# Performance work log

Hardware: AMD Instinct MI355X
Metric: run time of the kernel (lower is better)

## Reference

```python
import jax, jax.numpy as jnp
import numpy as np

DECAY = 0.1  # P['decay']


def setup_inputs() -> dict:
    key = jax.random.key(0)
    k0, k1, k2, k3, k4 = jax.random.split(key, 5)
    N, B, T = 512, 64, 1024
    hidden_0 = jax.random.normal(k0, (N,), dtype=jnp.float32)
    Batch_Input = jax.random.normal(k1, (B, T, N), dtype=jnp.float32)
    # scale recurrent weight ~1/sqrt(N) so the leaky-tanh dynamics stay bounded
    W = jax.random.normal(k2, (N, N), dtype=jnp.float32) / np.sqrt(N).astype(np.float32)
    Gw = jax.random.normal(k3, (2, N), dtype=jnp.float32)
    Gb = jax.random.normal(k4, (2,), dtype=jnp.float32)
    return {"hidden_0": hidden_0, "Batch_Input": Batch_Input, "W": W, "Gw": Gw, "Gb": Gb}


def reference(hidden_0, Batch_Input, W, Gw, Gb):
    B, T, N = Batch_Input.shape
    h0 = jnp.broadcast_to(hidden_0[None, :], (B, N))  # repeat over batch
    xs = jnp.swapaxes(Batch_Input, 0, 1)  # [T, B, N] for scan over time

    def step(h, x):
        # h_new = (1-d)*h + d*(tanh(h) @ W^T + x)   (einsum 'ab,cb->ca')
        h_new = (1.0 - DECAY) * h + DECAY * (jnp.tanh(h) @ W.T + x)
        return h_new, jnp.tanh(h_new)

    _, hidden_t = jax.lax.scan(step, h0, xs)  # hidden_t: [T, B, N]
    geometry = hidden_t @ Gw.T + Gb  # [T, B, 2]
    return jnp.swapaxes(hidden_t, 0, 1), jnp.swapaxes(geometry, 0, 1)
```

## Files before the change

### kernel.cpp

```cpp
#include <hip/hip_runtime.h>
#include <hip/hip_fp16.h>
#include <cmath>

#define RN 512
#define RT 1024
#define RB 64
#define SMEM_BYTES (131072 + 320)

typedef _Float16 half2v __attribute__((ext_vector_type(2)));

__device__ __forceinline__ float fast_tanh(float x) {
    float e = __expf(2.0f * x);
    return 1.0f - 2.0f / (e + 1.0f);
}
__device__ __forceinline__ unsigned pack2(float a, float b) {
    return (unsigned)__half_as_ushort(__float2half(a)) |
           ((unsigned)__half_as_ushort(__float2half(b)) << 16);
}
__device__ __forceinline__ unsigned pkrtz(float a, float b) {
    auto h = __builtin_amdgcn_cvt_pkrtz(a, b);
    return __builtin_bit_cast(unsigned, h);
}
__device__ __forceinline__ float dot2(unsigned wa, unsigned tb, float acc) {
    half2v a = __builtin_bit_cast(half2v, wa);
    half2v b = __builtin_bit_cast(half2v, tb);
    return __builtin_amdgcn_fdot2(a, b, acc, false);
}
template <int CTRL>
__device__ __forceinline__ float dpp_add(float x) {
    int p = __builtin_amdgcn_update_dpp(0, __float_as_int(x), CTRL, 0xf, 0xf, true);
    return x + __int_as_float(p);
}
__device__ __forceinline__ float red16(float x) {
    x = dpp_add<0xB1>(x);
    x = dpp_add<0x4E>(x);
    x = dpp_add<0x141>(x);
    x = dpp_add<0x140>(x);
    return x;
}
#define D2Q(acc, wq, tq) \
    acc = dot2((wq).x, (tq).x, acc); acc = dot2((wq).y, (tq).y, acc); \
    acc = dot2((wq).z, (tq).z, acc); acc = dot2((wq).w, (tq).w, acc);

__global__ void __launch_bounds__(512, 1) rnn_step_kernel(
    const float* __restrict__ h0,
    const float* __restrict__ X,
    const uint4* __restrict__ Wpk,
    const float* __restrict__ tanh0,
    float* __restrict__ outH,
    unsigned* __restrict__ ctr,
    unsigned* __restrict__ xcdctr)
{
    extern __shared__ unsigned char smem[];
    uint4*    Wl    = (uint4*)smem;
    unsigned* ownpk = (unsigned*)(smem + 131072);
    int*      bc    = (int*)(smem + 131072 + 256);
    unsigned* lctr  = (unsigned*)(smem + 131072 + 264);

    const int tid = threadIdx.x;
    if (tid == 0) {
        unsigned xcd;
        asm volatile("s_getreg_b32 %0, hwreg(HW_REG_XCC_ID)" : "=s"(xcd));
        xcd &= 7u;
        unsigned rank = __hip_atomic_fetch_add(&xcdctr[xcd], 1u,
                            __ATOMIC_RELAXED, __HIP_MEMORY_SCOPE_AGENT) & 31u;
        int slot = (int)(xcd * 32u + rank);
        bc[0] = slot >> 2;
        bc[1] = slot & 3;
        *lctr = 0u;
    }
    __syncthreads();
    const int batch = bc[0], part = bc[1];

    {
        const uint4* src = Wpk + part * 8192;
        #pragma unroll
        for (int i = 0; i < 16; ++i)
            Wl[i * 512 + tid] = src[i * 512 + tid];
    }

    const int rg = tid >> 4;
    const int kc = tid & 15;
    const int row0 = part * 128 + rg * 4;

    float4 h = {0, 0, 0, 0};
    float4 xv = {0, 0, 0, 0};
    if (kc == 0) {
        h = *reinterpret_cast<const float4*>(h0 + row0);
        float t0 = tanhf(h.x), t1 = tanhf(h.y), t2 = tanhf(h.z), t3 = tanhf(h.w);
        ownpk[2 * rg]     = pack2(t0, t1);
        ownpk[2 * rg + 1] = pack2(t2, t3);
        xv = *reinterpret_cast<const float4*>(&X[(size_t)batch * RT * RN + row0]);
    }

    unsigned* gctr = ctr + batch * 32;
    __syncthreads();

    #pragma unroll 1
    for (int t = 0; t < RT; ++t) {
        float4 xn = {0, 0, 0, 0};
        if (kc == 0) {
            const int tn = (t + 1 < RT) ? t + 1 : t;
            xn = *reinterpret_cast<const float4*>(&X[((size_t)batch * RT + tn) * RN + row0]);
        }

        float acc0 = 0.f, acc1 = 0.f, acc2 = 0.f, acc3 = 0.f;
        {
            uint4 th = *reinterpret_cast<const uint4*>(&ownpk[4 * kc]);
            uint4 wq0 = Wl[(part * 4 + 0) * 512 + tid];
            uint4 wq1 = Wl[(part * 4 + 1) * 512 + tid];
            uint4 wq2 = Wl[(part * 4 + 2) * 512 + tid];
            uint4 wq3 = Wl[(part * 4 + 3) * 512 + tid];
            D2Q(acc0, wq0, th) D2Q(acc1, wq1, th)
            D2Q(acc2, wq2, th) D2Q(acc3, wq3, th)
        }

        if (tid == 0 && t > 0) {
            const unsigned tgt = 4u * (unsigned)t;
            while (__hip_atomic_load(gctr, __ATOMIC_RELAXED,
                                     __HIP_MEMORY_SCOPE_AGENT) < tgt)
                __builtin_amdgcn_s_sleep(1);
        }
        __syncthreads();

        const float* srcR = (t == 0) ? tanh0
            : &outH[((size_t)batch * RT + (t - 1)) * RN];
        #pragma unroll
        for (int bb = 0; bb < 3; ++bb) {
            const int b = bb + (bb >= part);
            const int ko = b * 128 + kc * 8;
            float4 f0 = *reinterpret_cast<const float4*>(srcR + ko);
            float4 f1 = *reinterpret_cast<const float4*>(srcR + ko + 4);
            uint4 tv = make_uint4(pkrtz(f0.x, f0.y), pkrtz(f0.z, f0.w),
                                  pkrtz(f1.x, f1.y), pkrtz(f1.z, f1.w));
            uint4 wq0 = Wl[(b * 4 + 0) * 512 + tid];
            uint4 wq1 = Wl[(b * 4 + 1) * 512 + tid];
            uint4 wq2 = Wl[(b * 4 + 2) * 512 + tid];
            uint4 wq3 = Wl[(b * 4 + 3) * 512 + tid];
            D2Q(acc0, wq0, tv) D2Q(acc1, wq1, tv)
            D2Q(acc2, wq2, tv) D2Q(acc3, wq3, tv)
        }

        acc0 = red16(acc0); acc1 = red16(acc1);
        acc2 = red16(acc2); acc3 = red16(acc3);

        if (kc == 0) {
            h.x = 0.9f * h.x + 0.1f * (acc0 + xv.x);
            h.y = 0.9f * h.y + 0.1f * (acc1 + xv.y);
            h.z = 0.9f * h.z + 0.1f * (acc2 + xv.z);
            h.w = 0.9f * h.w + 0.1f * (acc3 + xv.w);
            float t0 = fast_tanh(h.x), t1 = fast_tanh(h.y);
            float t2 = fast_tanh(h.z), t3 = fast_tanh(h.w);
            *reinterpret_cast<float4*>(&outH[((size_t)batch * RT + t) * RN + row0]) =
                make_float4(t0, t1, t2, t3);
            ownpk[2 * rg]     = pack2(t0, t1);
            ownpk[2 * rg + 1] = pack2(t2, t3);
        }

        asm volatile("s_waitcnt vmcnt(0)" ::: "memory");
        if ((tid & 63) == 0) {
            unsigned a = __hip_atomic_fetch_add(lctr, 1u, __ATOMIC_RELAXED,
                                                __HIP_MEMORY_SCOPE_WORKGROUP);
            if ((a & 7u) == 7u)
                __hip_atomic_fetch_add(gctr, 1u, __ATOMIC_RELAXED,
                                       __HIP_MEMORY_SCOPE_AGENT);
        }
        __syncthreads();
        xv = xn;
    }
}

__global__ void pack_w(const float* __restrict__ W, uint4* __restrict__ Wpk)
{
    int o = blockIdx.x * blockDim.x + threadIdx.x;
    if (o >= 32768) return;
    int part = o >> 13;
    int b    = (o >> 11) & 3;
    int i    = (o >> 9) & 3;
    int tid  = o & 511;
    int row  = part * 128 + (tid >> 4) * 4 + i;
    int k0   = b * 128 + (tid & 15) * 8;
    const float* s = W + (size_t)row * RN + k0;
    uint4 v;
    v.x = pack2(s[0], s[1]); v.y = pack2(s[2], s[3]);
    v.z = pack2(s[4], s[5]); v.w = pack2(s[6], s[7]);
    Wpk[o] = v;
}

__global__ void geom_kernel(const float* __restrict__ hid,
                            const float* __restrict__ Gw,
                            const float* __restrict__ Gb,
                            float* __restrict__ geo)
{
    const int wid  = (blockIdx.x * blockDim.x + threadIdx.x) >> 6;
    const int lane = threadIdx.x & 63;
    if (wid >= RB * RT) return;
    const float* rowp = hid + (size_t)wid * RN;
    float g0 = 0.f, g1 = 0.f;
    #pragma unroll
    for (int j = 0; j < 8; ++j) {
        float v = rowp[lane + 64 * j];
        g0 = fmaf(v, Gw[lane + 64 * j], g0);
        g1 = fmaf(v, Gw[RN + lane + 64 * j], g1);
    }
    #pragma unroll
    for (int m = 32; m >= 1; m >>= 1) {
        g0 += __shfl_xor(g0, m);
        g1 += __shfl_xor(g1, m);
    }
    if (lane == 0) {
        geo[(size_t)wid * 2]     = g0 + Gb[0];
        geo[(size_t)wid * 2 + 1] = g1 + Gb[1];
    }
}

__global__ void init_misc(const float* __restrict__ h0,
                          float* __restrict__ tanh0,
                          unsigned* __restrict__ ctr,
                          unsigned* __restrict__ xcdctr)
{
    int i = blockIdx.x * blockDim.x + threadIdx.x;
    if (i < RN) tanh0[i] = tanhf(h0[i]);
    if (i < RB * 32) ctr[i] = 0u;
    if (i < 8) xcdctr[i] = 0u;
}

extern "C" void kernel_launch(void* const* d_in, const int* in_sizes, int n_in,
                              void* d_out, int out_size, void* d_ws, size_t ws_size,
                              hipStream_t stream)
{
    const float* h0 = (const float*)d_in[0];
    const float* X  = (const float*)d_in[1];
    const float* W  = (const float*)d_in[2];
    const float* Gw = (const float*)d_in[3];
    const float* Gb = (const float*)d_in[4];

    float* outH = (float*)d_out;
    float* geo  = outH + (size_t)RB * RT * RN;

    float*    tanh0  = (float*)d_ws;
    unsigned* ctr    = (unsigned*)d_ws + RN;
    unsigned* xcdctr = ctr + RB * 32;
    uint4*    Wpk    = (uint4*)(((uintptr_t)(xcdctr + 8) + 15) & ~(uintptr_t)15);

    (void)hipFuncSetAttribute((const void*)rnn_step_kernel,
                              hipFuncAttributeMaxDynamicSharedMemorySize, SMEM_BYTES);

    pack_w<<<64, 512, 0, stream>>>(W, Wpk);
    init_misc<<<8, 512, 0, stream>>>(h0, tanh0, ctr, xcdctr);

    void* kargs[] = { (void*)&h0, (void*)&X, (void*)&Wpk, (void*)&tanh0,
                      (void*)&outH, (void*)&ctr, (void*)&xcdctr };
    (void)hipLaunchCooperativeKernel(rnn_step_kernel, dim3(256), dim3(512),
                                     kargs, SMEM_BYTES, stream);

    geom_kernel<<<(RB * RT * 64 + 255) / 256, 256, 0, stream>>>(outH, Gw, Gb, geo);
}
```

Measured before the change: 2.034 ms.

## Process two batch rows per workgroup to reuse LDS weights and halve active blocks

Each workgroup now advances two batch sequences (b and b+32) at once, reusing each loaded weight fragment from LDS for two dot products. Only 16 of 32 launched blocks per XCD do work and the rest exit early, so 128 workgroups cover the 64 batches. This is meant to amortise LDS weight reads and the per-step barrier and spin-wait over twice the work. The cost is more compute, global loads and register pressure per step on each workgroup, plus reliance on the per-XCD rank assignment producing a valid mapping.

New measurement: 3.084 ms. +51.6%, slower.

```diff
diff --git a/kernel.cpp b/kernel.cpp
--- a/kernel.cpp
+++ b/kernel.cpp
@@ -5,7 +5,7 @@
 #define RN 512
 #define RT 1024
 #define RB 64
-#define SMEM_BYTES (131072 + 320)
+#define SMEM_BYTES (131072 + 1024)
 
 typedef _Float16 half2v __attribute__((ext_vector_type(2)));
 
@@ -54,8 +54,8 @@
     extern __shared__ unsigned char smem[];
     uint4*    Wl    = (uint4*)smem;
     unsigned* ownpk = (unsigned*)(smem + 131072);
-    int*      bc    = (int*)(smem + 131072 + 256);
-    unsigned* lctr  = (unsigned*)(smem + 131072 + 264);
+    int*      bc    = (int*)(smem + 131072 + 512);
+    unsigned* lctr  = (unsigned*)(smem + 131072 + 528);
 
     const int tid = threadIdx.x;
     if (tid == 0) {
@@ -64,13 +64,20 @@
         xcd &= 7u;
         unsigned rank = __hip_atomic_fetch_add(&xcdctr[xcd], 1u,
                             __ATOMIC_RELAXED, __HIP_MEMORY_SCOPE_AGENT) & 31u;
-        int slot = (int)(xcd * 32u + rank);
-        bc[0] = slot >> 2;
-        bc[1] = slot & 3;
+        if (rank < 16u) {
+            int slot = (int)(xcd * 16u + rank);
+            bc[0] = slot >> 2;
+            bc[1] = slot & 3;
+            bc[2] = 1;
+        } else {
+            bc[2] = 0;
+        }
         *lctr = 0u;
     }
     __syncthreads();
-    const int batch = bc[0], part = bc[1];
+    if (bc[2] == 0) return;
+    const int pair = bc[0], part = bc[1];
+    const int bA = pair, bB = pair + 32;
 
     {
         const uint4* src = Wpk + part * 8192;
@@ -83,36 +90,43 @@
     const int kc = tid & 15;
     const int row0 = part * 128 + rg * 4;
 
-    float4 h = {0, 0, 0, 0};
-    float4 xv = {0, 0, 0, 0};
+    float4 hA = {0,0,0,0}, hB = {0,0,0,0};
+    float4 xvA = {0,0,0,0}, xvB = {0,0,0,0};
     if (kc == 0) {
-        h = *reinterpret_cast<const float4*>(h0 + row0);
-        float t0 = tanhf(h.x), t1 = tanhf(h.y), t2 = tanhf(h.z), t3 = tanhf(h.w);
-        ownpk[2 * rg]     = pack2(t0, t1);
-        ownpk[2 * rg + 1] = pack2(t2, t3);
-        xv = *reinterpret_cast<const float4*>(&X[(size_t)batch * RT * RN + row0]);
-    }
-
-    unsigned* gctr = ctr + batch * 32;
+        hA = *reinterpret_cast<const float4*>(h0 + row0);
+        hB = hA;
+        float t0 = tanhf(hA.x), t1 = tanhf(hA.y), t2 = tanhf(hA.z), t3 = tanhf(hA.w);
+        ownpk[2 * rg]          = pack2(t0, t1);
+        ownpk[2 * rg + 1]      = pack2(t2, t3);
+        ownpk[64 + 2 * rg]     = pack2(t0, t1);
+        ownpk[64 + 2 * rg + 1] = pack2(t2, t3);
+        xvA = *reinterpret_cast<const float4*>(&X[(size_t)bA * RT * RN + row0]);
+        xvB = *reinterpret_cast<const float4*>(&X[(size_t)bB * RT * RN + row0]);
+    }
+
+    unsigned* gctr = ctr + pair * 32;
     __syncthreads();
 
     #pragma unroll 1
     for (int t = 0; t < RT; ++t) {
-        float4 xn = {0, 0, 0, 0};
+        float4 xnA = {0,0,0,0}, xnB = {0,0,0,0};
         if (kc == 0) {
             const int tn = (t + 1 < RT) ? t + 1 : t;
-            xn = *reinterpret_cast<const float4*>(&X[((size_t)batch * RT + tn) * RN + row0]);
-        }
-
-        float acc0 = 0.f, acc1 = 0.f, acc2 = 0.f, acc3 = 0.f;
+            xnA = *reinterpret_cast<const float4*>(&X[((size_t)bA * RT + tn) * RN + row0]);
+            xnB = *reinterpret_cast<const float4*>(&X[((size_t)bB * RT + tn) * RN + row0]);
+        }
+
+        float aA0 = 0.f, aA1 = 0.f, aA2 = 0.f, aA3 = 0.f;
+        float aB0 = 0.f, aB1 = 0.f, aB2 = 0.f, aB3 = 0.f;
         {
-            uint4 th = *reinterpret_cast<const uint4*>(&ownpk[4 * kc]);
+            uint4 thA = *reinterpret_cast<const uint4*>(&ownpk[4 * kc]);
+            uint4 thB = *reinterpret_cast<const uint4*>(&ownpk[64 + 4 * kc]);
             uint4 wq0 = Wl[(part * 4 + 0) * 512 + tid];
             uint4 wq1 = Wl[(part * 4 + 1) * 512 + tid];
             uint4 wq2 = Wl[(part * 4 + 2) * 512 + tid];
             uint4 wq3 = Wl[(part * 4 + 3) * 512 + tid];
-            D2Q(acc0, wq0, th) D2Q(acc1, wq1, th)
-            D2Q(acc2, wq2, th) D2Q(acc3, wq3, th)
+            D2Q(aA0, wq0, thA) D2Q(aA1, wq1, thA) D2Q(aA2, wq2, thA) D2Q(aA3, wq3, thA)
+            D2Q(aB0, wq0, thB) D2Q(aB1, wq1, thB) D2Q(aB2, wq2, thB) D2Q(aB3, wq3, thB)
         }
 
         if (tid == 0 && t > 0) {
@@ -123,38 +137,52 @@
         }
         __syncthreads();
 
-        const float* srcR = (t == 0) ? tanh0
-            : &outH[((size_t)batch * RT + (t - 1)) * RN];
+        const float* srcA = (t == 0) ? tanh0 : &outH[((size_t)bA * RT + (t - 1)) * RN];
+        const float* srcB = (t == 0) ? tanh0 : &outH[((size_t)bB * RT + (t - 1)) * RN];
         #pragma unroll
         for (int bb = 0; bb < 3; ++bb) {
             const int b = bb + (bb >= part);
             const int ko = b * 128 + kc * 8;
-            float4 f0 = *reinterpret_cast<const float4*>(srcR + ko);
-            float4 f1 = *reinterpret_cast<const float4*>(srcR + ko + 4);
-            uint4 tv = make_uint4(pkrtz(f0.x, f0.y), pkrtz(f0.z, f0.w),
-                                  pkrtz(f1.x, f1.y), pkrtz(f1.z, f1.w));
+            float4 fA0 = *reinterpret_cast<const float4*>(srcA + ko);
+            float4 fA1 = *reinterpret_cast<const float4*>(srcA + ko + 4);
+            float4 fB0 = *reinterpret_cast<const float4*>(srcB + ko);
+            float4 fB1 = *reinterpret_cast<const float4*>(srcB + ko + 4);
+            uint4 tvA = make_uint4(pkrtz(fA0.x, fA0.y), pkrtz(fA0.z, fA0.w),
+                                   pkrtz(fA1.x, fA1.y), pkrtz(fA1.z, fA1.w));
+            uint4 tvB = make_uint4(pkrtz(fB0.x, fB0.y), pkrtz(fB0.z, fB0.w),
+                                   pkrtz(fB1.x, fB1.y), pkrtz(fB1.z, fB1.w));
             uint4 wq0 = Wl[(b * 4 + 0) * 512 + tid];
             uint4 wq1 = Wl[(b * 4 + 1) * 512 + tid];
             uint4 wq2 = Wl[(b * 4 + 2) * 512 + tid];
             uint4 wq3 = Wl[(b * 4 + 3) * 512 + tid];
-            D2Q(acc0, wq0, tv) D2Q(acc1, wq1, tv)
-            D2Q(acc2, wq2, tv) D2Q(acc3, wq3, tv)
-        }
-
-        acc0 = red16(acc0); acc1 = red16(acc1);
-        acc2 = red16(acc2); acc3 = red16(acc3);
+            D2Q(aA0, wq0, tvA) D2Q(aA1, wq1, tvA) D2Q(aA2, wq2, tvA) D2Q(aA3, wq3, tvA)
+            D2Q(aB0, wq0, tvB) D2Q(aB1, wq1, tvB) D2Q(aB2, wq2, tvB) D2Q(aB3, wq3, tvB)
+        }
+
+        aA0 = red16(aA0); aA1 = red16(aA1); aA2 = red16(aA2); aA3 = red16(aA3);
+        aB0 = red16(aB0); aB1 = red16(aB1); aB2 = red16(aB2); aB3 = red16(aB3);
 
         if (kc == 0) {
-            h.x = 0.9f * h.x + 0.1f * (acc0 + xv.x);
-            h.y = 0.9f * h.y + 0.1f * (acc1 + xv.y);
-            h.z = 0.9f * h.z + 0.1f * (acc2 + xv.z);
-            h.w = 0.9f * h.w + 0.1f * (acc3 + xv.w);
-            float t0 = fast_tanh(h.x), t1 = fast_tanh(h.y);
-            float t2 = fast_tanh(h.z), t3 = fast_tanh(h.w);
-            *reinterpret_cast<float4*>(&outH[((size_t)batch * RT + t) * RN + row0]) =
-                make_float4(t0, t1, t2, t3);
-            ownpk[2 * rg]     = pack2(t0, t1);
-            ownpk[2 * rg + 1] = pack2(t2, t3);
+            hA.x = 0.9f * hA.x + 0.1f * (aA0 + xvA.x);
+            hA.y = 0.9f * hA.y + 0.1f * (aA1 + xvA.y);
+            hA.z = 0.9f * hA.z + 0.1f * (aA2 + xvA.z);
+            hA.w = 0.9f * hA.w + 0.1f * (aA3 + xvA.w);
+            hB.x = 0.9f * hB.x + 0.1f * (aB0 + xvB.x);
+            hB.y = 0.9f * hB.y + 0.1f * (aB1 + xvB.y);
+            hB.z = 0.9f * hB.z + 0.1f * (aB2 + xvB.z);
+            hB.w = 0.9f * hB.w + 0.1f * (aB3 + xvB.w);
+            float a0 = fast_tanh(hA.x), a1 = fast_tanh(hA.y);
+            float a2 = fast_tanh(hA.z), a3 = fast_tanh(hA.w);
+            float b0 = fast_tanh(hB.x), b1 = fast_tanh(hB.y);
+            float b2 = fast_tanh(hB.z), b3 = fast_tanh(hB.w);
+            *reinterpret_cast<float4*>(&outH[((size_t)bA * RT + t) * RN + row0]) =
+                make_float4(a0, a1, a2, a3);
+            *reinterpret_cast<float4*>(&outH[((size_t)bB * RT + t) * RN + row0]) =
+                make_float4(b0, b1, b2, b3);
+            ownpk[2 * rg]          = pack2(a0, a1);
+            ownpk[2 * rg + 1]      = pack2(a2, a3);
+            ownpk[64 + 2 * rg]     = pack2(b0, b1);
+            ownpk[64 + 2 * rg + 1] = pack2(b2, b3);
         }
 
         asm volatile("s_waitcnt vmcnt(0)" ::: "memory");
@@ -166,7 +194,7 @@
                                        __HIP_MEMORY_SCOPE_AGENT);
         }
         __syncthreads();
-        xv = xn;
+        xvA = xnA; xvB = xnB;
     }
 }
 
@@ -221,7 +249,7 @@
 {
     int i = blockIdx.x * blockDim.x + threadIdx.x;
     if (i < RN) tanh0[i] = tanhf(h0[i]);
-    if (i < RB * 32) ctr[i] = 0u;
+    if (i < 32 * 32) ctr[i] = 0u;
     if (i < 8) xcdctr[i] = 0u;
 }
 
@@ -240,7 +268,7 @@
 
     float*    tanh0  = (float*)d_ws;
     unsigned* ctr    = (unsigned*)d_ws + RN;
-    unsigned* xcdctr = ctr + RB * 32;
+    unsigned* xcdctr = ctr + 32 * 32;
     uint4*    Wpk    = (uint4*)(((uintptr_t)(xcdctr + 8) + 15) & ~(uintptr_t)15);
 
     (void)hipFuncSetAttribute((const void*)rnn_step_kernel,
```

## Switch recurrent matvec to column split with partial-sum exchange across blocks

Applied to the files above, without the earlier changes.

The recurrent matvec now gives each block a 128-column slice of W for all 512 output rows, using the block's own tanh values. Before, each block owned 128 rows and had to read the other blocks' tanh outputs after a barrier. Each block sends partial sums for the other blocks' rows through a double-buffered global exchange buffer, then reduces its own rows after the per-batch barrier. This removes the cross-lane DPP reduction and the dependent global reads of the other quarters' state before the matvec. It adds a global write and read of partial sums on every step and leaves only 64 threads to do the final update.

Result: slower. 2.540 ms (+24.9%).

```diff
diff --git a/kernel.cpp b/kernel.cpp
--- a/kernel.cpp
+++ b/kernel.cpp
@@ -5,7 +5,7 @@
 #define RN 512
 #define RT 1024
 #define RB 64
-#define SMEM_BYTES (131072 + 320)
+#define SMEM_BYTES 131872
 
 typedef _Float16 half2v __attribute__((ext_vector_type(2)));
 
@@ -16,28 +16,12 @@
 __device__ __forceinline__ unsigned pack2(float a, float b) {
     return (unsigned)__half_as_ushort(__float2half(a)) |
            ((unsigned)__half_as_ushort(__float2half(b)) << 16);
-}
-__device__ __forceinline__ unsigned pkrtz(float a, float b) {
-    auto h = __builtin_amdgcn_cvt_pkrtz(a, b);
-    return __builtin_bit_cast(unsigned, h);
 }
 __device__ __forceinline__ float dot2(unsigned wa, unsigned tb, float acc) {
     half2v a = __builtin_bit_cast(half2v, wa);
     half2v b = __builtin_bit_cast(half2v, tb);
     return __builtin_amdgcn_fdot2(a, b, acc, false);
 }
-template <int CTRL>
-__device__ __forceinline__ float dpp_add(float x) {
-    int p = __builtin_amdgcn_update_dpp(0, __float_as_int(x), CTRL, 0xf, 0xf, true);
-    return x + __int_as_float(p);
-}
-__device__ __forceinline__ float red16(float x) {
-    x = dpp_add<0xB1>(x);
-    x = dpp_add<0x4E>(x);
-    x = dpp_add<0x141>(x);
-    x = dpp_add<0x140>(x);
-    return x;
-}
 #define D2Q(acc, wq, tq) \
     acc = dot2((wq).x, (tq).x, acc); acc = dot2((wq).y, (tq).y, acc); \
     acc = dot2((wq).z, (tq).z, acc); acc = dot2((wq).w, (tq).w, acc);
@@ -46,16 +30,17 @@
     const float* __restrict__ h0,
     const float* __restrict__ X,
     const uint4* __restrict__ Wpk,
-    const float* __restrict__ tanh0,
     float* __restrict__ outH,
+    unsigned long long* __restrict__ exch,
     unsigned* __restrict__ ctr,
     unsigned* __restrict__ xcdctr)
 {
     extern __shared__ unsigned char smem[];
-    uint4*    Wl    = (uint4*)smem;
-    unsigned* ownpk = (unsigned*)(smem + 131072);
-    int*      bc    = (int*)(smem + 131072 + 256);
-    unsigned* lctr  = (unsigned*)(smem + 131072 + 264);
+    uint4*    Wl      = (uint4*)smem;
+    unsigned* ownpk   = (unsigned*)(smem + 131072);
+    float*    ownpart = (float*)(smem + 131072 + 256);
+    int*      bc      = (int*)(smem + 131072 + 768);
+    unsigned* lctr    = (unsigned*)(smem + 131072 + 776);
 
     const int tid = threadIdx.x;
     if (tid == 0) {
@@ -79,18 +64,12 @@
             Wl[i * 512 + tid] = src[i * 512 + tid];
     }
 
-    const int rg = tid >> 4;
-    const int kc = tid & 15;
-    const int row0 = part * 128 + rg * 4;
-
-    float4 h = {0, 0, 0, 0};
-    float4 xv = {0, 0, 0, 0};
-    if (kc == 0) {
-        h = *reinterpret_cast<const float4*>(h0 + row0);
-        float t0 = tanhf(h.x), t1 = tanhf(h.y), t2 = tanhf(h.z), t3 = tanhf(h.w);
-        ownpk[2 * rg]     = pack2(t0, t1);
-        ownpk[2 * rg + 1] = pack2(t2, t3);
-        xv = *reinterpret_cast<const float4*>(&X[(size_t)batch * RT * RN + row0]);
+    float2 hreg = {0.f, 0.f}, xv = {0.f, 0.f};
+    if (tid < 64) {
+        hreg = *reinterpret_cast<const float2*>(h0 + part * 128 + 2 * tid);
+        ownpk[tid] = pack2(tanhf(hreg.x), tanhf(hreg.y));
+        xv = *reinterpret_cast<const float2*>(
+            X + (size_t)batch * RT * RN + part * 128 + 2 * tid);
     }
 
     unsigned* gctr = ctr + batch * 32;
@@ -98,63 +77,38 @@
 
     #pragma unroll 1
     for (int t = 0; t < RT; ++t) {
-        float4 xn = {0, 0, 0, 0};
-        if (kc == 0) {
+        float2 xn = {0.f, 0.f};
+        if (tid < 64) {
             const int tn = (t + 1 < RT) ? t + 1 : t;
-            xn = *reinterpret_cast<const float4*>(&X[((size_t)batch * RT + tn) * RN + row0]);
-        }
-
-        float acc0 = 0.f, acc1 = 0.f, acc2 = 0.f, acc3 = 0.f;
+            xn = *reinterpret_cast<const float2*>(
+                X + ((size_t)batch * RT + tn) * RN + part * 128 + 2 * tid);
+        }
+
+        float acc = 0.f;
         {
-            uint4 th = *reinterpret_cast<const uint4*>(&ownpk[4 * kc]);
-            uint4 wq0 = Wl[(part * 4 + 0) * 512 + tid];
-            uint4 wq1 = Wl[(part * 4 + 1) * 512 + tid];
-            uint4 wq2 = Wl[(part * 4 + 2) * 512 + tid];
-            uint4 wq3 = Wl[(part * 4 + 3) * 512 + tid];
-            D2Q(acc0, wq0, th) D2Q(acc1, wq1, th)
-            D2Q(acc2, wq2, th) D2Q(acc3, wq3, th)
-        }
-
-        if (tid == 0 && t > 0) {
-            const unsigned tgt = 4u * (unsigned)t;
-            while (__hip_atomic_load(gctr, __ATOMIC_RELAXED,
-                                     __HIP_MEMORY_SCOPE_AGENT) < tgt)
-                __builtin_amdgcn_s_sleep(1);
-        }
-        __syncthreads();
-
-        const float* srcR = (t == 0) ? tanh0
-            : &outH[((size_t)batch * RT + (t - 1)) * RN];
-        #pragma unroll
-        for (int bb = 0; bb < 3; ++bb) {
-            const int b = bb + (bb >= part);
-            const int ko = b * 128 + kc * 8;
-            float4 f0 = *reinterpret_cast<const float4*>(srcR + ko);
-            float4 f1 = *reinterpret_cast<const float4*>(srcR + ko + 4);
-            uint4 tv = make_uint4(pkrtz(f0.x, f0.y), pkrtz(f0.z, f0.w),
-                                  pkrtz(f1.x, f1.y), pkrtz(f1.z, f1.w));
-            uint4 wq0 = Wl[(b * 4 + 0) * 512 + tid];
-            uint4 wq1 = Wl[(b * 4 + 1) * 512 + tid];
-            uint4 wq2 = Wl[(b * 4 + 2) * 512 + tid];
-            uint4 wq3 = Wl[(b * 4 + 3) * 512 + tid];
-            D2Q(acc0, wq0, tv) D2Q(acc1, wq1, tv)
-            D2Q(acc2, wq2, tv) D2Q(acc3, wq3, tv)
-        }
-
-        acc0 = red16(acc0); acc1 = red16(acc1);
-        acc2 = red16(acc2); acc3 = red16(acc3);
-
-        if (kc == 0) {
-            h.x = 0.9f * h.x + 0.1f * (acc0 + xv.x);
-            h.y = 0.9f * h.y + 0.1f * (acc1 + xv.y);
-            h.z = 0.9f * h.z + 0.1f * (acc2 + xv.z);
-            h.w = 0.9f * h.w + 0.1f * (acc3 + xv.w);
-            float t0 = fast_tanh(h.x), t1 = fast_tanh(h.y);
-            float t2 = fast_tanh(h.z), t3 = fast_tanh(h.w);
-            *reinterpret_cast<float4*>(&outH[((size_t)batch * RT + t) * RN + row0]) =
-                make_float4(t0, t1, t2, t3);
-            ownpk[2 * rg]     = pack2(t0, t1);
-            ownpk[2 * rg + 1] = pack2(t2, t3);
+            const uint4* wb = Wl + tid;
+            const uint4* tb = (const uint4*)ownpk;
+            #pragma unroll
+            for (int j = 0; j < 16; ++j) {
+                uint4 wq = wb[j * 512];
+                uint4 tq = tb[j];
+                D2Q(acc, wq, tq)
+            }
+        }
+        {
+            const int q = tid >> 7;
+            const float accp = __shfl_xor(acc, 1);
+            if (q == part) {
+                ownpart[tid & 127] = acc;
+            } else if (!(tid & 1)) {
+                const int s = (part < q) ? part : part - 1;
+                float2 pr = make_float2(acc, accp);
+                __hip_atomic_store(
+                    &exch[((((size_t)batch * 2 + (t & 1)) * 4 + q) * 3 + s) * 64
+                          + ((tid & 127) >> 1)],
+                    __builtin_bit_cast(unsigned long long, pr),
+                    __ATOMIC_RELAXED, __HIP_MEMORY_SCOPE_AGENT);
+            }
         }
 
         asm volatile("s_waitcnt vmcnt(0)" ::: "memory");
@@ -165,6 +119,38 @@
                 __hip_atomic_fetch_add(gctr, 1u, __ATOMIC_RELAXED,
                                        __HIP_MEMORY_SCOPE_AGENT);
         }
+        if (tid == 0) {
+            const unsigned tgt = 4u * (unsigned)(t + 1);
+            while (__hip_atomic_load(gctr, __ATOMIC_RELAXED,
+                                     __HIP_MEMORY_SCOPE_AGENT) < tgt)
+                __builtin_amdgcn_s_sleep(1);
+        }
+        __syncthreads();
+        asm volatile("" ::: "memory");
+
+        if (tid < 64) {
+            const unsigned long long* eb =
+                exch + (((size_t)batch * 2 + (t & 1)) * 4 + part) * 3 * 64;
+            unsigned long long u0 = __hip_atomic_load(eb + 0 * 64 + tid,
+                                        __ATOMIC_RELAXED, __HIP_MEMORY_SCOPE_AGENT);
+            unsigned long long u1 = __hip_atomic_load(eb + 1 * 64 + tid,
+                                        __ATOMIC_RELAXED, __HIP_MEMORY_SCOPE_AGENT);
+            unsigned long long u2 = __hip_atomic_load(eb + 2 * 64 + tid,
+                                        __ATOMIC_RELAXED, __HIP_MEMORY_SCOPE_AGENT);
+            float2 p0 = __builtin_bit_cast(float2, u0);
+            float2 p1 = __builtin_bit_cast(float2, u1);
+            float2 p2 = __builtin_bit_cast(float2, u2);
+            float2 own = *reinterpret_cast<const float2*>(ownpart + 2 * tid);
+            float d0 = own.x + p0.x + p1.x + p2.x;
+            float d1 = own.y + p0.y + p1.y + p2.y;
+            hreg.x = 0.9f * hreg.x + 0.1f * (d0 + xv.x);
+            hreg.y = 0.9f * hreg.y + 0.1f * (d1 + xv.y);
+            const float th0 = fast_tanh(hreg.x), th1 = fast_tanh(hreg.y);
+            *reinterpret_cast<float2*>(
+                outH + ((size_t)batch * RT + t) * RN + part * 128 + 2 * tid) =
+                make_float2(th0, th1);
+            ownpk[tid] = pack2(th0, th1);
+        }
         __syncthreads();
         xv = xn;
     }
@@ -175,12 +161,9 @@
     int o = blockIdx.x * blockDim.x + threadIdx.x;
     if (o >= 32768) return;
     int part = o >> 13;
-    int b    = (o >> 11) & 3;
-    int i    = (o >> 9) & 3;
+    int j    = (o >> 9) & 15;
     int tid  = o & 511;
-    int row  = part * 128 + (tid >> 4) * 4 + i;
-    int k0   = b * 128 + (tid & 15) * 8;
-    const float* s = W + (size_t)row * RN + k0;
+    const float* s = W + (size_t)tid * RN + part * 128 + j * 8;
     uint4 v;
     v.x = pack2(s[0], s[1]); v.y = pack2(s[2], s[3]);
     v.z = pack2(s[4], s[5]); v.w = pack2(s[6], s[7]);
@@ -214,13 +197,10 @@
     }
 }
 
-__global__ void init_misc(const float* __restrict__ h0,
-                          float* __restrict__ tanh0,
-                          unsigned* __restrict__ ctr,
+__global__ void init_misc(unsigned* __restrict__ ctr,
                           unsigned* __restrict__ xcdctr)
 {
     int i = blockIdx.x * blockDim.x + threadIdx.x;
-    if (i < RN) tanh0[i] = tanhf(h0[i]);
     if (i < RB * 32) ctr[i] = 0u;
     if (i < 8) xcdctr[i] = 0u;
 }
@@ -238,8 +218,8 @@
     float* outH = (float*)d_out;
     float* geo  = outH + (size_t)RB * RT * RN;
 
-    float*    tanh0  = (float*)d_ws;
-    unsigned* ctr    = (unsigned*)d_ws + RN;
+    unsigned long long* exch = (unsigned long long*)d_ws;
+    unsigned* ctr    = (unsigned*)(exch + (size_t)RB * 2 * 4 * 3 * 64);
     unsigned* xcdctr = ctr + RB * 32;
     uint4*    Wpk    = (uint4*)(((uintptr_t)(xcdctr + 8) + 15) & ~(uintptr_t)15);
 
@@ -247,10 +227,10 @@
                               hipFuncAttributeMaxDynamicSharedMemorySize, SMEM_BYTES);
 
     pack_w<<<64, 512, 0, stream>>>(W, Wpk);
-    init_misc<<<8, 512, 0, stream>>>(h0, tanh0, ctr, xcdctr);
-
-    void* kargs[] = { (void*)&h0, (void*)&X, (void*)&Wpk, (void*)&tanh0,
-                      (void*)&outH, (void*)&ctr, (void*)&xcdctr };
+    init_misc<<<8, 512, 0, stream>>>(ctr, xcdctr);
+
+    void* kargs[] = { (void*)&h0, (void*)&X, (void*)&Wpk,
+                      (void*)&outH, (void*)&exch, (void*)&ctr, (void*)&xcdctr };
     (void)hipLaunchCooperativeKernel(rnn_step_kernel, dim3(256), dim3(512),
                                      kargs, SMEM_BYTES, stream);
 
```

## Split recurrent matmul by input columns and exchange fp16 partial sums

Applied to the files above, without the earlier changes.

Adds a column-partitioned recurrent kernel. Each of the four blocks per batch holds a 128-column slice of W and computes partial products for all 512 outputs from its own tanh slice. The other blocks' partials are sent as packed fp16 through a per-timestep global exchange buffer and reduced after one counter barrier. Because the exchange buffer is indexed per timestep, no buffer reuse is needed. The goal is to stop each block from gathering the full 512-wide tanh state from global memory every step. In exchange it writes and reads partial sums each step, rounds partials to fp16, and needs a large workspace. The old row kernel remains as a fallback when the workspace is too small.

Result: slower. 2.363 ms (+16.2%).

```diff
diff --git a/kernel.cpp b/kernel.cpp
--- a/kernel.cpp
+++ b/kernel.cpp
@@ -5,7 +5,8 @@
 #define RN 512
 #define RT 1024
 #define RB 64
-#define SMEM_BYTES (131072 + 320)
+#define SMEM_COL 131872
+#define SMEM_ROW (131072 + 320)
 
 typedef _Float16 half2v __attribute__((ext_vector_type(2)));
 
@@ -20,6 +21,12 @@
 __device__ __forceinline__ unsigned pkrtz(float a, float b) {
     auto h = __builtin_amdgcn_cvt_pkrtz(a, b);
     return __builtin_bit_cast(unsigned, h);
+}
+__device__ __forceinline__ float h16lo(unsigned u) {
+    return __half2float(__ushort_as_half((unsigned short)(u & 0xffffu)));
+}
+__device__ __forceinline__ float h16hi(unsigned u) {
+    return __half2float(__ushort_as_half((unsigned short)(u >> 16)));
 }
 __device__ __forceinline__ float dot2(unsigned wa, unsigned tb, float acc) {
     half2v a = __builtin_bit_cast(half2v, wa);
@@ -42,7 +49,141 @@
     acc = dot2((wq).x, (tq).x, acc); acc = dot2((wq).y, (tq).y, acc); \
     acc = dot2((wq).z, (tq).z, acc); acc = dot2((wq).w, (tq).w, acc);
 
-__global__ void __launch_bounds__(512, 1) rnn_step_kernel(
+__global__ void __launch_bounds__(512, 1) rnn_col_kernel(
+    const float* __restrict__ h0,
+    const float* __restrict__ X,
+    const uint4* __restrict__ Wpk,
+    float* __restrict__ outH,
+    unsigned* __restrict__ exch,
+    unsigned* __restrict__ ctr,
+    unsigned* __restrict__ xcdctr)
+{
+    extern __shared__ unsigned char smem[];
+    uint4*    Wl      = (uint4*)smem;
+    unsigned* ownpk   = (unsigned*)(smem + 131072);
+    float*    ownpart = (float*)(smem + 131072 + 256);
+    int*      bc      = (int*)(smem + 131072 + 768);
+    unsigned* lctr    = (unsigned*)(smem + 131072 + 776);
+
+    const int tid = threadIdx.x;
+    if (tid == 0) {
+        unsigned xcd;
+        asm volatile("s_getreg_b32 %0, hwreg(HW_REG_XCC_ID)" : "=s"(xcd));
+        xcd &= 7u;
+        unsigned rank = __hip_atomic_fetch_add(&xcdctr[xcd], 1u,
+                            __ATOMIC_RELAXED, __HIP_MEMORY_SCOPE_AGENT) & 31u;
+        int slot = (int)(xcd * 32u + rank);
+        bc[0] = slot >> 2;
+        bc[1] = slot & 3;
+        *lctr = 0u;
+    }
+    __syncthreads();
+    const int batch = bc[0], part = bc[1];
+
+    {
+        const uint4* src = Wpk + part * 8192;
+        #pragma unroll
+        for (int i = 0; i < 16; ++i)
+            Wl[i * 512 + tid] = src[i * 512 + tid];
+    }
+
+    float2 hreg = {0.f, 0.f}, xv = {0.f, 0.f};
+    if (tid < 64) {
+        hreg = *reinterpret_cast<const float2*>(h0 + part * 128 + 2 * tid);
+        ownpk[tid] = pack2(tanhf(hreg.x), tanhf(hreg.y));
+        xv = *reinterpret_cast<const float2*>(
+            X + (size_t)batch * RT * RN + part * 128 + 2 * tid);
+    }
+
+    unsigned* gctr = ctr + batch * 32;
+    __syncthreads();
+
+    #pragma unroll 1
+    for (int t = 0; t < RT; ++t) {
+        float2 xn = {0.f, 0.f};
+        if (tid < 64) {
+            const int tn = (t + 1 < RT) ? t + 1 : t;
+            xn = *reinterpret_cast<const float2*>(
+                X + ((size_t)batch * RT + tn) * RN + part * 128 + 2 * tid);
+        }
+
+        float acc = 0.f;
+        {
+            const uint4* wb = Wl + tid;
+            const uint4* tb = (const uint4*)ownpk;
+            #pragma unroll
+            for (int j = 0; j < 16; ++j) {
+                uint4 wq = wb[j * 512];
+                uint4 tq = tb[j];
+                D2Q(acc, wq, tq)
+            }
+        }
+        {
+            const float accp = __shfl_xor(acc, 1);
+            const int q = tid >> 7;
+            if (q == part) {
+                ownpart[tid & 127] = acc;
+            } else if (!(tid & 1)) {
+                const int s = (part < q) ? part : part - 1;
+                exch[(((size_t)batch * RT + t) * 4 + q) * 192
+                     + s * 64 + ((tid & 127) >> 1)] = pack2(acc, accp);
+            }
+        }
+
+        asm volatile("s_waitcnt vmcnt(0)" ::: "memory");
+        if ((tid & 63) == 0) {
+            unsigned a = __hip_atomic_fetch_add(lctr, 1u, __ATOMIC_RELAXED,
+                                                __HIP_MEMORY_SCOPE_WORKGROUP);
+            if ((a & 7u) == 7u)
+                __hip_atomic_fetch_add(gctr, 1u, __ATOMIC_RELAXED,
+                                       __HIP_MEMORY_SCOPE_AGENT);
+        }
+        if (tid == 0) {
+            const unsigned tgt = 4u * (unsigned)(t + 1);
+            while (__hip_atomic_load(gctr, __ATOMIC_RELAXED,
+                                     __HIP_MEMORY_SCOPE_AGENT) < tgt)
+                __builtin_amdgcn_s_sleep(1);
+        }
+        __syncthreads();
+        asm volatile("" ::: "memory");
+
+        if (tid < 64) {
+            const unsigned* eb =
+                exch + (((size_t)batch * RT + t) * 4 + part) * 192;
+            unsigned u0 = eb[0 * 64 + tid];
+            unsigned u1 = eb[1 * 64 + tid];
+            unsigned u2 = eb[2 * 64 + tid];
+            float2 own = *reinterpret_cast<const float2*>(ownpart + 2 * tid);
+            float d0 = own.x + h16lo(u0) + h16lo(u1) + h16lo(u2);
+            float d1 = own.y + h16hi(u0) + h16hi(u1) + h16hi(u2);
+            hreg.x = 0.9f * hreg.x + 0.1f * (d0 + xv.x);
+            hreg.y = 0.9f * hreg.y + 0.1f * (d1 + xv.y);
+            const float th0 = fast_tanh(hreg.x), th1 = fast_tanh(hreg.y);
+            *reinterpret_cast<float2*>(
+                outH + ((size_t)batch * RT + t) * RN + part * 128 + 2 * tid) =
+                make_float2(th0, th1);
+            ownpk[tid] = pack2(th0, th1);
+        }
+        __syncthreads();
+        xv = xn;
+    }
+}
+
+__global__ void pack_w_col(const float* __restrict__ W, uint4* __restrict__ Wpk)
+{
+    int o = blockIdx.x * blockDim.x + threadIdx.x;
+    if (o >= 32768) return;
+    int part = o >> 13;
+    int j    = (o >> 9) & 15;
+    int tid  = o & 511;
+    const float* s = W + (size_t)tid * RN + part * 128 + j * 8;
+    uint4 v;
+    v.x = pack2(s[0], s[1]); v.y = pack2(s[2], s[3]);
+    v.z = pack2(s[4], s[5]); v.w = pack2(s[6], s[7]);
+    Wpk[o] = v;
+}
+
+__global__ void __launch_bounds__(512, 1) rnn_row_kernel(
     const float* __restrict__ h0,
     const float* __restrict__ X,
     const uint4* __restrict__ Wpk,
@@ -170,7 +311,7 @@
     }
 }
 
-__global__ void pack_w(const float* __restrict__ W, uint4* __restrict__ Wpk)
+__global__ void pack_w_row(const float* __restrict__ W, uint4* __restrict__ Wpk)
 {
     int o = blockIdx.x * blockDim.x + threadIdx.x;
     if (o >= 32768) return;
@@ -238,21 +379,41 @@
     float* outH = (float*)d_out;
     float* geo  = outH + (size_t)RB * RT * RN;
 
-    float*    tanh0  = (float*)d_ws;
-    unsigned* ctr    = (unsigned*)d_ws + RN;
-    unsigned* xcdctr = ctr + RB * 32;
-    uint4*    Wpk    = (uint4*)(((uintptr_t)(xcdctr + 8) + 15) & ~(uintptr_t)15);
-
-    (void)hipFuncSetAttribute((const void*)rnn_step_kernel,
-                              hipFuncAttributeMaxDynamicSharedMemorySize, SMEM_BYTES);
-
-    pack_w<<<64, 512, 0, stream>>>(W, Wpk);
-    init_misc<<<8, 512, 0, stream>>>(h0, tanh0, ctr, xcdctr);
-
-    void* kargs[] = { (void*)&h0, (void*)&X, (void*)&Wpk, (void*)&tanh0,
-                      (void*)&outH, (void*)&ctr, (void*)&xcdctr };
-    (void)hipLaunchCooperativeKernel(rnn_step_kernel, dim3(256), dim3(512),
-                                     kargs, SMEM_BYTES, stream);
+    const size_t exch_u32 = (size_t)RB * RT * 4 * 192;
+    const size_t need_fast = exch_u32 * 4 + (RN + RB * 32 + 8) * 4 + 64 + 524288;
+
+    if (ws_size >= need_fast) {
+        unsigned* exch   = (unsigned*)d_ws;
+        float*    tanh0  = (float*)(exch + exch_u32);
+        unsigned* ctr    = (unsigned*)(tanh0 + RN);
+        unsigned* xcdctr = ctr + RB * 32;
+        uint4*    Wpk    = (uint4*)(((uintptr_t)(xcdctr + 8) + 63) & ~(uintptr_t)63);
+
+        (void)hipFuncSetAttribute((const void*)rnn_col_kernel,
+                                  hipFuncAttributeMaxDynamicSharedMemorySize, SMEM_COL);
+        pack_w_col<<<64, 512, 0, stream>>>(W, Wpk);
+        init_misc<<<8, 512, 0, stream>>>(h0, tanh0, ctr, xcdctr);
+
+        void* kargs[] = { (void*)&h0, (void*)&X, (void*)&Wpk,
+                          (void*)&outH, (void*)&exch, (void*)&ctr, (void*)&xcdctr };
+        (void)hipLaunchCooperativeKernel(rnn_col_kernel, dim3(256), dim3(512),
+                                         kargs, SMEM_COL, stream);
+    } else {
+        float*    tanh0  = (float*)d_ws;
+        unsigned* ctr    = (unsigned*)d_ws + RN;
+        unsigned* xcdctr = ctr + RB * 32;
+        uint4*    Wpk    = (uint4*)(((uintptr_t)(xcdctr + 8) + 63) & ~(uintptr_t)63);
+
+        (void)hipFuncSetAttribute((const void*)rnn_row_kernel,
+                                  hipFuncAttributeMaxDynamicSharedMemorySize, SMEM_ROW);
+        pack_w_row<<<64, 512, 0, stream>>>(W, Wpk);
+        init_misc<<<8, 512, 0, stream>>>(h0, tanh0, ctr, xcdctr);
+
+        void* kargs[] = { (void*)&h0, (void*)&X, (void*)&Wpk, (void*)&tanh0,
+                          (void*)&outH, (void*)&ctr, (void*)&xcdctr };
+        (void)hipLaunchCooperativeKernel(rnn_row_kernel, dim3(256), dim3(512),
+                                         kargs, SMEM_ROW, stream);
+    }
 
     geom_kernel<<<(RB * RT * 64 + 255) / 256, 256, 0, stream>>>(outH, Gw, Gb, geo);
 }
```
